# Kernel optimization log

Hardware: AMD Instinct MI355X
Metric: run time of the kernel (lower is better)

## Reference

```python
import jax, jax.numpy as jnp
import numpy as np

# Note: the original applies F.dropout(p=0.2) after the shared Linear. Dropout is
# omitted here (identity) so the reference is deterministic; this is the eval-mode math.

def setup_inputs() -> dict:
    key = jax.random.key(0)
    k1, k2, k3 = jax.random.split(key, 3)
    B, L, D = 8, 2048, 1024  # D = dim*4 with dim=256
    ix = jax.random.normal(k1, (B, L, D), dtype=jnp.float32)
    iother = jax.random.normal(k2, (B, L, D), dtype=jnp.float32)
    # Linear(dim*4, dim*4) weight/bias, torch convention W: [out, in]
    W = jax.random.normal(k3, (D, D), dtype=jnp.float32) * (1.0 / np.sqrt(D))
    b = jnp.zeros((D,), dtype=jnp.float32)
    return {"ix": ix, "iother": iother, "W": W, "b": b}


def reference(ix, iother, W, b):
    # shared projection (torch Linear: x @ W.T + b)
    ex = ix @ W.T + b            # [B, Lx, D]
    eother = iother @ W.T + b    # [B, Lo, D]
    # cross-attention scores (no scaling, per original)
    align = jnp.einsum('bld,bmd->blm', ex, eother)   # [B, Lx, Lo]
    align = jax.nn.softmax(align, axis=-1)
    # note: values are the RAW iother, not the projected eother
    aligned = jnp.einsum('blm,bmd->bld', align, iother)  # [B, Lx, D]
    return aligned
```

## Files before the change

### kernel.cpp

```cpp
#include <hip/hip_runtime.h>
#include <stdint.h>
#include <stddef.h>


typedef short bf16x8 __attribute__((ext_vector_type(8)));
typedef float f32x4  __attribute__((ext_vector_type(4)));

typedef const __attribute__((address_space(1))) uint32_t* gas_ptr;
typedef __attribute__((address_space(3))) uint32_t* las_ptr;

__device__ __forceinline__ void gl_lds16(const void* g, void* l) {
    __builtin_amdgcn_global_load_lds((gas_ptr)g, (las_ptr)l, 16, 0, 0);
}

__device__ __forceinline__ unsigned short f2bf(float f) {
    union { float f; uint32_t u; } v; v.f = f;
    uint32_t r = v.u + 0x7fffu + ((v.u >> 16) & 1u);
    return (unsigned short)(r >> 16);
}
__device__ __forceinline__ float bf2f(unsigned short h) {
    union { uint32_t u; float f; } v; v.u = ((uint32_t)h) << 16; return v.f;
}

#define L_ 2048
#define D_ 1024
#define ROWB 4096
#define NKT 32
#define SLOT 49152
#define LDSB 32768
#define DYN_LDS (3 * SLOT)

__global__ __launch_bounds__(256) void k_split(
        const float* __restrict__ in, unsigned short* __restrict__ hl, int n4) {
    const int i = blockIdx.x * 256 + threadIdx.x;
    if (i >= n4) return;
    float4 v = ((const float4*)in)[i];
    unsigned short h0 = f2bf(v.x), h1 = f2bf(v.y), h2 = f2bf(v.z), h3 = f2bf(v.w);
    unsigned short l0 = f2bf(v.x - bf2f(h0)), l1 = f2bf(v.y - bf2f(h1));
    unsigned short l2 = f2bf(v.z - bf2f(h2)), l3 = f2bf(v.w - bf2f(h3));
    uint2 hu, lu;
    hu.x = (uint32_t)h0 | ((uint32_t)h1 << 16);
    hu.y = (uint32_t)h2 | ((uint32_t)h3 << 16);
    lu.x = (uint32_t)l0 | ((uint32_t)l1 << 16);
    lu.y = (uint32_t)l2 | ((uint32_t)l3 << 16);
    const int row = i >> 8;
    const int c4 = (i & 255) << 2;
    const size_t o = (size_t)row * 2048 + ((c4 >> 5) << 6) + (c4 & 31);
    *(uint2*)&hl[o]      = hu;
    *(uint2*)&hl[o + 32] = lu;
}

__global__ __launch_bounds__(256) void k_transpose(
        const float* __restrict__ V, unsigned short* __restrict__ Vt) {
    __shared__ unsigned short tile[64][72];
    const int b = blockIdx.z, k0 = blockIdx.x * 64, n0 = blockIdx.y * 64;
    const int t = threadIdx.x;
    const int row = t >> 2, cs = (t & 3) * 16;
    const float* src = V + ((size_t)b * L_ + k0 + row) * D_ + n0 + cs;
#pragma unroll
    for (int q = 0; q < 4; q++) {
        float4 f = ((const float4*)src)[q];
        tile[row][cs + q * 4 + 0] = f2bf(f.x);
        tile[row][cs + q * 4 + 1] = f2bf(f.y);
        tile[row][cs + q * 4 + 2] = f2bf(f.z);
        tile[row][cs + q * 4 + 3] = f2bf(f.w);
    }
    __syncthreads();
    union { unsigned short us[16]; uint4 q[2]; } pk;
#pragma unroll
    for (int j = 0; j < 16; j++) pk.us[j] = tile[cs + j][row];
    unsigned short* dst = Vt + ((size_t)b * D_ + n0 + row) * L_ + k0 + cs;
    *(uint4*)dst       = pk.q[0];
    *(uint4*)(dst + 8) = pk.q[1];
}

__global__ __launch_bounds__(256) void k_tsplit(
        const float* __restrict__ W, unsigned short* __restrict__ Wt) {
    __shared__ float tile[64][68];
    const int n0 = blockIdx.x * 64, k0 = blockIdx.y * 64;
    const int t = threadIdx.x;
    const int row = t >> 2, cs = (t & 3) * 16;
    const float* src = W + ((size_t)(n0 + row)) * D_ + k0 + cs;
#pragma unroll
    for (int q = 0; q < 4; q++) {
        float4 f = ((const float4*)src)[q];
        tile[row][cs + q * 4 + 0] = f.x;
        tile[row][cs + q * 4 + 1] = f.y;
        tile[row][cs + q * 4 + 2] = f.z;
        tile[row][cs + q * 4 + 3] = f.w;
    }
    __syncthreads();
    union { unsigned short us[16]; uint4 q[2]; } hi, lo;
#pragma unroll
    for (int j = 0; j < 16; j++) {
        float v = tile[cs + j][row];
        unsigned short h = f2bf(v);
        hi.us[j] = h;
        lo.us[j] = f2bf(v - bf2f(h));
    }
    const int ng = n0 + cs;
    unsigned short* dst = Wt + (size_t)(k0 + row) * 2048 + ((ng >> 5) << 6) + (ng & 31);
    *(uint4*)dst        = hi.q[0];
    *(uint4*)(dst + 8)  = hi.q[1];
    *(uint4*)(dst + 32) = lo.q[0];
    *(uint4*)(dst + 40) = lo.q[1];
}

struct Frg { bf16x8 aH[4], aL[4], bH[4], bL[4]; };

template<int SP3>
__device__ __forceinline__ void mfma_cluster(const Frg& f, f32x4 (&acc)[4][4]) {
    __builtin_amdgcn_s_setprio(1);
#pragma unroll
    for (int i = 0; i < 4; i++)
#pragma unroll
        for (int j = 0; j < 4; j++) {
            f32x4 c = acc[i][j];
            if (SP3) {
                c = __builtin_amdgcn_mfma_f32_16x16x32_bf16(f.aH[i], f.bH[j], c, 0, 0, 0);
                c = __builtin_amdgcn_mfma_f32_16x16x32_bf16(f.aH[i], f.bL[j], c, 0, 0, 0);
                c = __builtin_amdgcn_mfma_f32_16x16x32_bf16(f.aL[i], f.bH[j], c, 0, 0, 0);
            } else {
                c = __builtin_amdgcn_mfma_f32_16x16x32_bf16(f.aH[i], f.bH[j], c, 0, 0, 0);
                c = __builtin_amdgcn_mfma_f32_16x16x32_bf16(f.aL[i], f.bL[j], c, 0, 0, 0);
            }
            acc[i][j] = c;
        }
    __builtin_amdgcn_s_setprio(0);
}

template<int SP3>
__device__ __forceinline__ void gemm_mainloop(
        const char* __restrict__ Ag, const char* __restrict__ Bg,
        f32x4 (&acc)[4][4], int kt0, int nkt) {
    extern __shared__ char smem[];
    const int t = threadIdx.x, lane = t & 63, w = t >> 6;
    const int l16 = lane & 15, quad = lane >> 4;
    const int mw = w >> 1, nw = w & 1;
    const int ln8 = lane >> 3, l8 = lane & 7;

    const int scol = (l8 * 16) ^ (ln8 << 4);
    const char* gA = Ag + (size_t)(w * 8 + ln8) * ROWB + scol;
    const char* gB = Bg + (size_t)(w * 8 + ln8) * ROWB + scol;
    const int sdst = w * 1024;

    const int swz  = (l16 & 7) << 4;
    const int colH = (quad * 16) ^ swz;
    const int colL = (64 + quad * 16) ^ swz;
    const int aRow = (mw * 64 + l16) * 128;
    const int bRow = LDSB + (nw * 64 + l16) * 128;

#pragma unroll
    for (int i = 0; i < 4; i++)
#pragma unroll
        for (int j = 0; j < 4; j++) acc[i][j] = (f32x4){0.f, 0.f, 0.f, 0.f};

    auto STAGE = [&](int soff, int ktAbs) {
        char* sb = smem + soff;
        const size_t gko = (size_t)ktAbs * 128;
#pragma unroll
        for (int q = 0; q < 4; q++)
            gl_lds16(gA + (size_t)q * (64 * ROWB) + gko, sb + q * 8192 + sdst);
#pragma unroll
        for (int q = 0; q < 2; q++)
            gl_lds16(gB + (size_t)q * (64 * ROWB) + gko, sb + LDSB + q * 8192 + sdst);
    };
    auto LDF = [&](int soff, Frg& f) {
        const char* cb = smem + soff;
#pragma unroll
        for (int i = 0; i < 4; i++) {
            const int ro = aRow + i * 2048;
            f.aH[i] = *(const bf16x8*)(cb + ro + colH);
            f.aL[i] = *(const bf16x8*)(cb + ro + colL);
        }
#pragma unroll
        for (int j = 0; j < 4; j++) {
            const int ro = bRow + j * 2048;
            f.bH[j] = *(const bf16x8*)(cb + ro + colH);
            f.bL[j] = *(const bf16x8*)(cb + ro + colL);
        }
    };

    STAGE(0, kt0 + 0);
    STAGE(SLOT, kt0 + 1);
    asm volatile("s_waitcnt vmcnt(6)" ::: "memory");
    __builtin_amdgcn_s_barrier();
    Frg fC, fN;
    LDF(0, fC);

    int ktr = 2 & (nkt - 1), sCur = 0;
#pragma unroll 1
    for (int it = 0; it < nkt / 2; ++it) {
        {
            int sStage = sCur + 2 * SLOT; if (sStage >= 3 * SLOT) sStage -= 3 * SLOT;
            int sLd    = sCur + SLOT;     if (sLd    >= 3 * SLOT) sLd    -= 3 * SLOT;
            STAGE(sStage, kt0 + ktr); ktr = (ktr + 1) & (nkt - 1);
            asm volatile("s_waitcnt vmcnt(6)" ::: "memory");
            asm volatile("s_waitcnt lgkmcnt(0)" ::: "memory");
            __builtin_amdgcn_s_barrier();
            LDF(sLd, fN);
            mfma_cluster<SP3>(fC, acc);
            sCur = sLd;
        }
        {
            int sStage = sCur + 2 * SLOT; if (sStage >= 3 * SLOT) sStage -= 3 * SLOT;
            int sLd    = sCur + SLOT;     if (sLd    >= 3 * SLOT) sLd    -= 3 * SLOT;
            STAGE(sStage, kt0 + ktr); ktr = (ktr + 1) & (nkt - 1);
            asm volatile("s_waitcnt vmcnt(6)" ::: "memory");
            asm volatile("s_waitcnt lgkmcnt(0)" ::: "memory");
            __builtin_amdgcn_s_barrier();
            LDF(sLd, fC);
            mfma_cluster<SP3>(fN, acc);
            sCur = sLd;
        }
    }
}

__global__ __launch_bounds__(512, 2) void k_wtw(
        const char* __restrict__ Wt, float* __restrict__ Mpart, int nkt) {
    const int M0 = blockIdx.x * 256, N0 = blockIdx.y * 128, z = blockIdx.z;
    f32x4 acc[4][4];
    gemm_mainloop<1>(Wt + (size_t)M0 * ROWB, Wt + (size_t)N0 * ROWB, acc, z * nkt, nkt);

    const int t = threadIdx.x, lane = t & 63, w = t >> 6;
    const int l16 = lane & 15, quad = lane >> 4, mw = w >> 1, nw = w & 1;
    float* Sp = Mpart + ((size_t)z << 20)
              + (size_t)(M0 + mw * 64 + quad * 4) * 1024 + N0 + nw * 64;
#pragma unroll
    for (int i = 0; i < 4; i++)
#pragma unroll
        for (int j = 0; j < 4; j++)
#pragma unroll
            for (int r = 0; r < 4; r++)
                Sp[(size_t)(i * 16 + r) * 1024 + j * 16 + l16] = acc[i][j][r];
}

__global__ __launch_bounds__(256) void k_mreduce(
        const float* __restrict__ Mpart, unsigned short* __restrict__ Mhl, int zn) {
    const int i = blockIdx.x;
    const int j = threadIdx.x * 4;
    float4 s = {0.f, 0.f, 0.f, 0.f};
    for (int z = 0; z < zn; z++) {
        float4 v = *(const float4*)(Mpart + ((size_t)z << 20) + (size_t)i * 1024 + j);
        s.x += v.x; s.y += v.y; s.z += v.z; s.w += v.w;
    }
    unsigned short h0 = f2bf(s.x), h1 = f2bf(s.y), h2 = f2bf(s.z), h3 = f2bf(s.w);
    unsigned short l0 = f2bf(s.x - bf2f(h0)), l1 = f2bf(s.y - bf2f(h1));
    unsigned short l2 = f2bf(s.z - bf2f(h2)), l3 = f2bf(s.w - bf2f(h3));
    uint2 hu, lu;
    hu.x = (uint32_t)h0 | ((uint32_t)h1 << 16);
    hu.y = (uint32_t)h2 | ((uint32_t)h3 << 16);
    lu.x = (uint32_t)l0 | ((uint32_t)l1 << 16);
    lu.y = (uint32_t)l2 | ((uint32_t)l3 << 16);
    const size_t o = (size_t)i * 2048 + ((j >> 5) << 6) + (j & 31);
    *(uint2*)&Mhl[o]      = hu;
    *(uint2*)&Mhl[o + 32] = lu;
}

__global__ __launch_bounds__(256) void k_wtb(
        const float* __restrict__ W, const float* __restrict__ b,
        float* __restrict__ c) {
    const int k = blockIdx.x * 256 + threadIdx.x;
    const int n0 = blockIdx.y * 128;
    float s = 0.f;
#pragma unroll 4
    for (int n = 0; n < 128; n++) s += b[n0 + n] * W[(size_t)(n0 + n) * D_ + k];
    atomicAdd(&c[k], s);
}

__global__ __launch_bounds__(256) void k_v2(
        const float* __restrict__ io, const float* __restrict__ c,
        float* __restrict__ v2) {
    __shared__ float cs[1024];
    const int t = threadIdx.x;
#pragma unroll
    for (int q = 0; q < 4; q++) cs[q * 256 + t] = c[q * 256 + t];
    __syncthreads();
    const int r = blockIdx.x * 4 + (t >> 6);
    const int lane = t & 63;
    const float* row = io + (size_t)r * D_ + lane * 16;
    float s = 0.f;
#pragma unroll
    for (int q = 0; q < 4; q++) {
        float4 v = ((const float4*)row)[q];
        s += v.x * cs[lane * 16 + q * 4 + 0] + v.y * cs[lane * 16 + q * 4 + 1]
           + v.z * cs[lane * 16 + q * 4 + 2] + v.w * cs[lane * 16 + q * 4 + 3];
    }
#pragma unroll
    for (int o = 32; o > 0; o >>= 1) s += __shfl_xor(s, o, 64);
    if (lane == 0) v2[r] = s;
}

__global__ __launch_bounds__(512, 2) void k_gproj(
        const char* __restrict__ Ahl, const char* __restrict__ Mhl,
        unsigned short* __restrict__ Ehl) {
    const int M0 = blockIdx.x * 256, N0 = blockIdx.y * 128;
    f32x4 acc[4][4];
    gemm_mainloop<1>(Ahl + (size_t)M0 * ROWB, Mhl + (size_t)N0 * ROWB, acc, 0, NKT);

    const int t = threadIdx.x, lane = t & 63, w = t >> 6;
    const int l16 = lane & 15, quad = lane >> 4, mw = w >> 1, nw = w & 1;
#pragma unroll
    for (int j = 0; j < 4; j++) {
        const int n = N0 + nw * 64 + j * 16 + l16;
        unsigned short* eb = Ehl + (size_t)(M0 + mw * 64 + quad * 4) * 2048
                             + (size_t)(n >> 5) * 64 + (n & 31);
#pragma unroll
        for (int i = 0; i < 4; i++)
#pragma unroll
            for (int r = 0; r < 4; r++) {
                float v = acc[i][j][r];
                unsigned short h  = f2bf(v);
                unsigned short lo = f2bf(v - bf2f(h));
                unsigned short* p = eb + (size_t)(i * 16 + r) * 2048;
                p[0]  = h;
                p[32] = lo;
            }
    }
}

__global__ __launch_bounds__(512, 2) void k_gscores(
        const char* __restrict__ Ehl, const char* __restrict__ Ohl,
        const float* __restrict__ v2, float* __restrict__ S) {
    const int M0 = blockIdx.x * 256, N0 = blockIdx.y * 128, bb = blockIdx.z;
    const char* Ae = Ehl + (size_t)(bb * L_ + M0) * ROWB;
    const char* Be = Ohl + (size_t)(bb * L_ + N0) * ROWB;
    f32x4 acc[4][4];
    gemm_mainloop<1>(Ae, Be, acc, 0, NKT);

    const int t = threadIdx.x, lane = t & 63, w = t >> 6;
    const int l16 = lane & 15, quad = lane >> 4, mw = w >> 1, nw = w & 1;
    float* Sp = S + ((size_t)bb * L_ + M0 + mw * 64 + quad * 4) * (size_t)L_
                  + N0 + nw * 64;
    const float* v2p = v2 + (size_t)bb * L_ + N0 + nw * 64;
#pragma unroll
    for (int j = 0; j < 4; j++) {
        const float vb = v2p[j * 16 + l16];
#pragma unroll
        for (int i = 0; i < 4; i++)
#pragma unroll
            for (int r = 0; r < 4; r++)
                Sp[(size_t)(i * 16 + r) * L_ + j * 16 + l16] = acc[i][j][r] + vb;
    }
}

__global__ __launch_bounds__(256) void k_rowsoftmax(
        const float* __restrict__ S, unsigned short* __restrict__ P) {
    const size_t r = blockIdx.x;
    const float* row = S + r * (size_t)L_;
    const int t = threadIdx.x, lane = t & 63, wave = t >> 6;
    float4 v0 = ((const float4*)row)[t];
    float4 v1 = ((const float4*)row)[t + 256];
    float mx = fmaxf(fmaxf(fmaxf(v0.x, v0.y), fmaxf(v0.z, v0.w)),
                     fmaxf(fmaxf(v1.x, v1.y), fmaxf(v1.z, v1.w)));
#pragma unroll
    for (int o = 32; o > 0; o >>= 1) mx = fmaxf(mx, __shfl_xor(mx, o, 64));
    __shared__ float red[4];
    __shared__ float bmax, binv;
    if (lane == 0) red[wave] = mx;
    __syncthreads();
    if (t == 0) bmax = fmaxf(fmaxf(red[0], red[1]), fmaxf(red[2], red[3]));
    __syncthreads();
    const float m = bmax;
    float e0x = __expf(fminf(v0.x - m, 0.f)), e0y = __expf(fminf(v0.y - m, 0.f));
    float e0z = __expf(fminf(v0.z - m, 0.f)), e0w = __expf(fminf(v0.w - m, 0.f));
    float e1x = __expf(fminf(v1.x - m, 0.f)), e1y = __expf(fminf(v1.y - m, 0.f));
    float e1z = __expf(fminf(v1.z - m, 0.f)), e1w = __expf(fminf(v1.w - m, 0.f));
    float s = e0x + e0y + e0z + e0w + e1x + e1y + e1z + e1w;
#pragma unroll
    for (int o = 32; o > 0; o >>= 1) s += __shfl_xor(s, o, 64);
    __syncthreads();
    if (lane == 0) red[wave] = s;
    __syncthreads();
    if (t == 0) binv = 1.0f / (red[0] + red[1] + red[2] + red[3]);
    __syncthreads();
    const float ril = binv;
    uint2 a, b;
    a.x = (uint32_t)f2bf(e0x * ril) | ((uint32_t)f2bf(e0y * ril) << 16);
    a.y = (uint32_t)f2bf(e0z * ril) | ((uint32_t)f2bf(e0w * ril) << 16);
    b.x = (uint32_t)f2bf(e1x * ril) | ((uint32_t)f2bf(e1y * ril) << 16);
    b.y = (uint32_t)f2bf(e1z * ril) | ((uint32_t)f2bf(e1w * ril) << 16);
    uint2* pr = (uint2*)(P + r * (size_t)L_);
    pr[t]       = a;
    pr[t + 256] = b;
}

__global__ __launch_bounds__(512, 2) void k_pvg(
        const char* __restrict__ Pbf, const char* __restrict__ Vt,
        float* __restrict__ out) {
    const int M0 = blockIdx.x * 256, N0 = blockIdx.y * 128, bb = blockIdx.z;
    const char* Ae = Pbf + ((size_t)bb * L_ + M0) * ROWB;
    const char* Be = Vt + ((size_t)bb * D_ + N0) * ROWB;
    f32x4 acc[4][4];
    gemm_mainloop<0>(Ae, Be, acc, 0, NKT);

    const int t = threadIdx.x, lane = t & 63, w = t >> 6;
    const int l16 = lane & 15, quad = lane >> 4, mw = w >> 1, nw = w & 1;
    float* op = out + ((size_t)bb * L_ + M0 + mw * 64 + quad * 4) * (size_t)D_
                    + N0 + nw * 64;
#pragma unroll
    for (int i = 0; i < 4; i++)
#pragma unroll
        for (int j = 0; j < 4; j++)
#pragma unroll
            for (int r = 0; r < 4; r++)
                op[(size_t)(i * 16 + r) * D_ + j * 16 + l16] = acc[i][j][r];
}

extern "C" void kernel_launch(void* const* d_in, const int* in_sizes, int n_in,
                              void* d_out, int out_size, void* d_ws, size_t ws_size,
                              hipStream_t stream) {
    const float* ix   = (const float*)d_in[0];
    const float* io   = (const float*)d_in[1];
    const float* W    = (const float*)d_in[2];
    const float* bias = (const float*)d_in[3];
    float* out = (float*)d_out;

    hipFuncSetAttribute((const void*)k_gproj,
                        hipFuncAttributeMaxDynamicSharedMemorySize, DYN_LDS);
    hipFuncSetAttribute((const void*)k_gscores,
                        hipFuncAttributeMaxDynamicSharedMemorySize, DYN_LDS);
    hipFuncSetAttribute((const void*)k_wtw,
                        hipFuncAttributeMaxDynamicSharedMemorySize, DYN_LDS);
    hipFuncSetAttribute((const void*)k_pvg,
                        hipFuncAttributeMaxDynamicSharedMemorySize, DYN_LDS);

    const size_t MB = 1024 * 1024;
    const size_t PB_EI = (size_t)L_ * ROWB;
    const size_t PB_S  = (size_t)L_ * L_ * 4;
    const size_t PB_E  = (size_t)L_ * D_ * 2;
    const size_t PB_ST = (size_t)L_ * 4;

    int nb = 8;
    while (nb > 1) {
        size_t need = 4 * MB + (size_t)nb * (2 * PB_EI + PB_S + PB_E + 2 * PB_ST) + 8192;
        if (need <= ws_size) break;
        nb >>= 1;
    }

    char* ws = (char*)d_ws;
    size_t off = 0;
    unsigned short* Mhl = (unsigned short*)(ws + off); off += 4 * MB;
    unsigned short* EHL = (unsigned short*)(ws + off); off += (size_t)nb * PB_EI;
    unsigned short* OHL = (unsigned short*)(ws + off); off += (size_t)nb * PB_EI;
    char* regA = ws + off;                             off += (size_t)nb * PB_S;
    unsigned short* Vt = (unsigned short*)(ws + off);  off += (size_t)nb * PB_E;
    float* v2   = (float*)(ws + off);                  off += (size_t)nb * PB_ST;
    float* cvec = (float*)(ws + off);                  off += 4096;
    unsigned short* WtHL = EHL;
    float* Mpart = (float*)OHL;
    unsigned short* Pbf = EHL;
    const int zsplit = (nb >= 2) ? 8 : 4;
    const int nktc = NKT / zsplit;

    k_tsplit<<<dim3(16, 16), 256, 0, stream>>>(W, WtHL);
    k_wtw<<<dim3(4, 8, zsplit), 512, DYN_LDS, stream>>>((const char*)WtHL, Mpart, nktc);
    k_mreduce<<<1024, 256, 0, stream>>>(Mpart, Mhl, zsplit);
    hipMemsetAsync(cvec, 0, D_ * sizeof(float), stream);
    k_wtb<<<dim3(4, 8), 256, 0, stream>>>(W, bias, cvec);

    for (int b0 = 0; b0 < 8; b0 += nb) {
        const float* ixc = ix + (size_t)b0 * L_ * D_;
        const float* ioc = io + (size_t)b0 * L_ * D_;
        float* outc = out + (size_t)b0 * L_ * D_;
        const int nLD4 = nb * L_ * D_ / 4;
        const int nbL = nb * L_;
        float* S = (float*)regA;

        k_split<<<nb * 2048, 256, 0, stream>>>(ixc, (unsigned short*)regA, nLD4);
        k_split<<<nb * 2048, 256, 0, stream>>>(ioc, OHL, nLD4);
        k_transpose<<<dim3(32, 16, nb), 256, 0, stream>>>(ioc, Vt);
        k_v2<<<nbL / 4, 256, 0, stream>>>(ioc, cvec, v2);
        k_gproj<<<dim3(nbL / 256, D_ / 128), 512, DYN_LDS, stream>>>(
            (const char*)regA, (const char*)Mhl, EHL);
        k_gscores<<<dim3(L_ / 256, L_ / 128, nb), 512, DYN_LDS, stream>>>(
            (const char*)EHL, (const char*)OHL, v2, S);
        k_rowsoftmax<<<2048 * nb, 256, 0, stream>>>(S, Pbf);
        k_pvg<<<dim3(L_ / 256, D_ / 128, nb), 512, DYN_LDS, stream>>>(
            (const char*)Pbf, (const char*)Vt, outc);
    }
}
```

Baseline: 613.7 us.

## Use 256x256 tiles with double-buffered mainloop for scores GEMM and XCD-aware block remap

Adds a new GEMM mainloop with a 256x256 output tile (8 waves in a 2x4 layout, each holding 8x4 accumulators) and two 64 KB LDS buffers, used for the split-bf16 scores GEMM. The larger tile raises arithmetic intensity per byte loaded. Block indices for the scores and PV kernels are also remapped so that consecutive tiles land on the same XCD, which should improve L2 reuse. In exchange, the bigger tile doubles accumulator registers and uses 128 KB of LDS, which may cap occupancy at one block per CU despite the launch bound of 2. The simpler two-stage pipeline, with full waits at each stage, may also expose more latency.

New measurement: 605.2 us. No clear change (-1.4%).

```diff
diff --git a/kernel.cpp b/kernel.cpp
--- a/kernel.cpp
+++ b/kernel.cpp
@@ -29,6 +29,20 @@
 #define SLOT 49152
 #define LDSB 32768
 #define DYN_LDS (3 * SLOT)
+#define SLOT2 65536
+#define LDSB2 32768
+#define DYN_LDS2 (2 * SLOT2)
+
+__device__ __forceinline__ void xcd_remap(int gx, int gy, int& m, int& n, int& z) {
+    const int bid = blockIdx.x + gx * (blockIdx.y + gy * blockIdx.z);
+    const int T = gx * gy * (int)gridDim.z;
+    const int chunk = T >> 3;
+    const int b2 = (bid & 7) * chunk + (bid >> 3);
+    m = b2 % gx;
+    const int r = b2 / gx;
+    n = r % gy;
+    z = r / gy;
+}
 
 __global__ __launch_bounds__(256) void k_split(
         const float* __restrict__ in, unsigned short* __restrict__ hl, int n4) {
@@ -216,6 +230,93 @@
     }
 }
 
+__device__ __forceinline__ void gemm_mainloop2(
+        const char* __restrict__ Ag, const char* __restrict__ Bg,
+        f32x4 (&acc)[8][4]) {
+    extern __shared__ char smem[];
+    const int t = threadIdx.x, lane = t & 63, w = t >> 6;
+    const int l16 = lane & 15, quad = lane >> 4;
+    const int mw = w >> 2, nw = w & 3;
+    const int ln8 = lane >> 3, l8 = lane & 7;
+
+    const int scol = (l8 * 16) ^ (ln8 << 4);
+    const char* gA = Ag + (size_t)(w * 8 + ln8) * ROWB + scol;
+    const char* gB = Bg + (size_t)(w * 8 + ln8) * ROWB + scol;
+    const int sdst = w * 1024;
+
+    const int swz  = (l16 & 7) << 4;
+    const int colH = (quad * 16) ^ swz;
+    const int colL = (64 + quad * 16) ^ swz;
+    const int aRow = (mw * 128 + l16) * 128;
+    const int bRow = LDSB2 + (nw * 64 + l16) * 128;
+
+#pragma unroll
+    for (int i = 0; i < 8; i++)
+#pragma unroll
+        for (int j = 0; j < 4; j++) acc[i][j] = (f32x4){0.f, 0.f, 0.f, 0.f};
+
+    auto STAGE = [&](int soff, int ktAbs) {
+        char* sb = smem + soff;
+        const size_t gko = (size_t)ktAbs * 128;
+#pragma unroll
+        for (int q = 0; q < 4; q++)
+            gl_lds16(gA + (size_t)q * (64 * ROWB) + gko, sb + q * 8192 + sdst);
+#pragma unroll
+        for (int q = 0; q < 4; q++)
+            gl_lds16(gB + (size_t)q * (64 * ROWB) + gko, sb + LDSB2 + q * 8192 + sdst);
+    };
+    auto COMPUTE = [&](int soff) {
+        const char* cb = smem + soff;
+        bf16x8 bH[4], bL[4];
+#pragma unroll
+        for (int j = 0; j < 4; j++) {
+            const int ro = bRow + j * 2048;
+            bH[j] = *(const bf16x8*)(cb + ro + colH);
+            bL[j] = *(const bf16x8*)(cb + ro + colL);
+        }
+#pragma unroll
+        for (int h = 0; h < 2; h++) {
+            bf16x8 aH[4], aL[4];
+#pragma unroll
+            for (int i = 0; i < 4; i++) {
+                const int ro = aRow + h * 8192 + i * 2048;
+                aH[i] = *(const bf16x8*)(cb + ro + colH);
+                aL[i] = *(const bf16x8*)(cb + ro + colL);
+            }
+            __builtin_amdgcn_s_setprio(1);
+#pragma unroll
+            for (int i = 0; i < 4; i++)
+#pragma unroll
+                for (int j = 0; j < 4; j++) {
+                    f32x4 c = acc[h * 4 + i][j];
+                    c = __builtin_amdgcn_mfma_f32_16x16x32_bf16(aH[i], bH[j], c, 0, 0, 0);
+                    c = __builtin_amdgcn_mfma_f32_16x16x32_bf16(aH[i], bL[j], c, 0, 0, 0);
+                    c = __builtin_amdgcn_mfma_f32_16x16x32_bf16(aL[i], bH[j], c, 0, 0, 0);
+                    acc[h * 4 + i][j] = c;
+                }
+            __builtin_amdgcn_s_setprio(0);
+        }
+    };
+
+    STAGE(0, 0);
+    int ktn = 1;
+#pragma unroll 1
+    for (int it = 0; it < NKT / 2; ++it) {
+        STAGE(SLOT2, ktn); ktn = (ktn + 1) & (NKT - 1);
+        asm volatile("s_waitcnt vmcnt(8)" ::: "memory");
+        __builtin_amdgcn_s_barrier();
+        COMPUTE(0);
+        asm volatile("s_waitcnt lgkmcnt(0)" ::: "memory");
+        __builtin_amdgcn_s_barrier();
+        STAGE(0, ktn); ktn = (ktn + 1) & (NKT - 1);
+        asm volatile("s_waitcnt vmcnt(8)" ::: "memory");
+        __builtin_amdgcn_s_barrier();
+        COMPUTE(SLOT2);
+        asm volatile("s_waitcnt lgkmcnt(0)" ::: "memory");
+        __builtin_amdgcn_s_barrier();
+    }
+}
+
 __global__ __launch_bounds__(512, 2) void k_wtw(
         const char* __restrict__ Wt, float* __restrict__ Mpart, int nkt) {
     const int M0 = blockIdx.x * 256, N0 = blockIdx.y * 128, z = blockIdx.z;
@@ -322,22 +423,24 @@
 __global__ __launch_bounds__(512, 2) void k_gscores(
         const char* __restrict__ Ehl, const char* __restrict__ Ohl,
         const float* __restrict__ v2, float* __restrict__ S) {
-    const int M0 = blockIdx.x * 256, N0 = blockIdx.y * 128, bb = blockIdx.z;
+    int mb, nb_, zb;
+    xcd_remap(L_ / 256, L_ / 256, mb, nb_, zb);
+    const int M0 = mb * 256, N0 = nb_ * 256, bb = zb;
     const char* Ae = Ehl + (size_t)(bb * L_ + M0) * ROWB;
     const char* Be = Ohl + (size_t)(bb * L_ + N0) * ROWB;
-    f32x4 acc[4][4];
-    gemm_mainloop<1>(Ae, Be, acc, 0, NKT);
+    f32x4 acc[8][4];
+    gemm_mainloop2(Ae, Be, acc);
 
     const int t = threadIdx.x, lane = t & 63, w = t >> 6;
-    const int l16 = lane & 15, quad = lane >> 4, mw = w >> 1, nw = w & 1;
-    float* Sp = S + ((size_t)bb * L_ + M0 + mw * 64 + quad * 4) * (size_t)L_
+    const int l16 = lane & 15, quad = lane >> 4, mw = w >> 2, nw = w & 3;
+    float* Sp = S + ((size_t)bb * L_ + M0 + mw * 128 + quad * 4) * (size_t)L_
                   + N0 + nw * 64;
     const float* v2p = v2 + (size_t)bb * L_ + N0 + nw * 64;
 #pragma unroll
     for (int j = 0; j < 4; j++) {
         const float vb = v2p[j * 16 + l16];
 #pragma unroll
-        for (int i = 0; i < 4; i++)
+        for (int i = 0; i < 8; i++)
 #pragma unroll
             for (int r = 0; r < 4; r++)
                 Sp[(size_t)(i * 16 + r) * L_ + j * 16 + l16] = acc[i][j][r] + vb;
@@ -388,7 +491,9 @@
 __global__ __launch_bounds__(512, 2) void k_pvg(
         const char* __restrict__ Pbf, const char* __restrict__ Vt,
         float* __restrict__ out) {
-    const int M0 = blockIdx.x * 256, N0 = blockIdx.y * 128, bb = blockIdx.z;
+    int mb, nb_, zb;
+    xcd_remap(L_ / 256, D_ / 128, mb, nb_, zb);
+    const int M0 = mb * 256, N0 = nb_ * 128, bb = zb;
     const char* Ae = Pbf + ((size_t)bb * L_ + M0) * ROWB;
     const char* Be = Vt + ((size_t)bb * D_ + N0) * ROWB;
     f32x4 acc[4][4];
@@ -419,7 +524,7 @@
     hipFuncSetAttribute((const void*)k_gproj,
                         hipFuncAttributeMaxDynamicSharedMemorySize, DYN_LDS);
     hipFuncSetAttribute((const void*)k_gscores,
-                        hipFuncAttributeMaxDynamicSharedMemorySize, DYN_LDS);
+                        hipFuncAttributeMaxDynamicSharedMemorySize, DYN_LDS2);
     hipFuncSetAttribute((const void*)k_wtw,
                         hipFuncAttributeMaxDynamicSharedMemorySize, DYN_LDS);
     hipFuncSetAttribute((const void*)k_pvg,
@@ -473,7 +578,7 @@
         k_v2<<<nbL / 4, 256, 0, stream>>>(ioc, cvec, v2);
         k_gproj<<<dim3(nbL / 256, D_ / 128), 512, DYN_LDS, stream>>>(
             (const char*)regA, (const char*)Mhl, EHL);
-        k_gscores<<<dim3(L_ / 256, L_ / 128, nb), 512, DYN_LDS, stream>>>(
+        k_gscores<<<dim3(L_ / 256, L_ / 256, nb), 512, DYN_LDS2, stream>>>(
             (const char*)EHL, (const char*)OHL, v2, S);
         k_rowsoftmax<<<2048 * nb, 256, 0, stream>>>(S, Pbf);
         k_pvg<<<dim3(L_ / 256, D_ / 128, nb), 512, DYN_LDS, stream>>>(
```
